# Optimization experiments

Measured on AMD Instinct MI355X. Metric: run time of the kernel, lower is better.

## Reference

```python
import jax, jax.numpy as jnp
import numpy as np

D_MODEL = 64
LN_EPS = 1e-5


def _conv1d(x, w, b, stride, pad):
    # x: (B, Cin, L), w: (Cout, Cin, K)
    y = jax.lax.conv_general_dilated(x, w, (stride,), [(pad, pad)],
                                     dimension_numbers=('NCH', 'OIH', 'NCH'))
    return y + b[None, :, None]


def _layernorm(x, g, b):
    # normalize over last dim (feature dim), matching nn.LayerNorm(d_model)
    m = jnp.mean(x, axis=-1, keepdims=True)
    v = jnp.var(x, axis=-1, keepdims=True)
    return (x - m) * jax.lax.rsqrt(v + LN_EPS) * g + b


def _pos_embed(L, d):
    pos = jnp.arange(L, dtype=jnp.float32)[:, None]
    div = jnp.exp(jnp.arange(0, d, 2, dtype=jnp.float32) * (-np.log(10000.0) / d))
    pe = jnp.zeros((L, d), jnp.float32)
    pe = pe.at[:, 0::2].set(jnp.sin(pos * div))
    pe = pe.at[:, 1::2].set(jnp.cos(pos * div))
    return pe


def setup_inputs():
    key = jax.random.key(0)
    ks = jax.random.split(key, 20)
    B, L, D = 128, 4096, D_MODEL
    G = D // 4  # 16 convs per kernel-size group (kernels cycle [3,5,7,9])
    inp = {'x': jax.random.normal(ks[0], (B, 1, L), jnp.float32)}
    kernels = [3, 5, 7, 9]
    for i, k in enumerate(kernels):
        fan = float(1.0 / np.sqrt(k))
        inp['tok_w%d' % k] = jax.random.uniform(ks[1 + 2 * i], (G, 1, k), jnp.float32, -fan, fan)
        inp['tok_b%d' % k] = jax.random.uniform(ks[2 + 2 * i], (G,), jnp.float32, -fan, fan)
    fan = float(1.0 / np.sqrt(D * 4))
    for j in range(3):
        inp['c_w%d' % (j + 1)] = jax.random.uniform(ks[10 + 2 * j], (D, D, 4), jnp.float32, -fan, fan)
        inp['c_b%d' % (j + 1)] = jax.random.uniform(ks[11 + 2 * j], (D,), jnp.float32, -fan, fan)
    for j in range(2):
        inp['ln_g%d' % (j + 1)] = jnp.ones((D,), jnp.float32)
        inp['ln_b%d' % (j + 1)] = jnp.zeros((D,), jnp.float32)
    return inp


def reference(x, tok_w3, tok_b3, tok_w5, tok_b5, tok_w7, tok_b7, tok_w9, tok_b9,
              c_w1, c_b1, c_w2, c_b2, c_w3, c_b3, ln_g1, ln_b1, ln_g2, ln_b2):
    B, _, L = x.shape
    D = D_MODEL
    # TokenEmbedding: conv i has kernel [3,5,7,9][i%4]; fuse the d_model 1-channel
    # convs into 4 grouped convs (one per kernel size), then interleave channels.
    outs = [
        _conv1d(x, tok_w3, tok_b3, 1, 1),
        _conv1d(x, tok_w5, tok_b5, 1, 2),
        _conv1d(x, tok_w7, tok_b7, 1, 3),
        _conv1d(x, tok_w9, tok_b9, 1, 4),
    ]  # each (B, D//4, L); group g holds channels i with i % 4 == g, ordered by i // 4
    emb = jnp.stack(outs, axis=2).reshape(B, D, L)  # channel i = (i//4)*4 + (i%4)
    # add sinusoidal positional embedding (dropout is identity in eval mode)
    h = emb + _pos_embed(L, D).T[None]  # (B, D, L)
    # CompressionEmbedding: conv(k=4, s=2, p=1) -> tanh -> LN (over D) chain
    h = jnp.tanh(_conv1d(h, c_w1, c_b1, 2, 1))
    h = _layernorm(h.transpose(0, 2, 1), ln_g1, ln_b1).transpose(0, 2, 1)
    h = jnp.tanh(_conv1d(h, c_w2, c_b2, 2, 1))
    h = _layernorm(h.transpose(0, 2, 1), ln_g2, ln_b2).transpose(0, 2, 1)
    h = jnp.tanh(_conv1d(h, c_w3, c_b3, 2, 1))
    return h.transpose(0, 2, 1)  # (B, L//8, D)
```

## Files before the change

kernel.cpp:

```cpp
#include <hip/hip_runtime.h>
#include <math.h>

#define BATCH 128
#define LN_EPS 1e-5f

typedef short bf16x8 __attribute__((ext_vector_type(8)));
typedef short bf16x4 __attribute__((ext_vector_type(4)));
typedef float f32x4  __attribute__((ext_vector_type(4)));

__device__ __forceinline__ ushort f2bf(float f) {
    return __builtin_bit_cast(ushort, (__bf16)f);
}

__device__ __forceinline__ float fast_tanh(float v) {
    float e = __expf(2.f * v);
    return 1.f - 2.f / (e + 1.f);
}

__global__ __launch_bounds__(256, 2)
void prep_kernel(const float* __restrict__ cw1, const float* __restrict__ cw2,
                 const float* __restrict__ cw3,
                 const float* __restrict__ w3, const float* __restrict__ b3,
                 const float* __restrict__ w5, const float* __restrict__ b5,
                 const float* __restrict__ w7, const float* __restrict__ b7,
                 const float* __restrict__ w9, const float* __restrict__ b9,
                 const float* __restrict__ cb1, const float* __restrict__ cb2,
                 const float* __restrict__ cb3,
                 const float* __restrict__ lg1, const float* __restrict__ lb1,
                 const float* __restrict__ lg2, const float* __restrict__ lb2,
                 ushort* __restrict__ Wm23, ushort* __restrict__ Wm1,
                 float* __restrict__ W0c, float* __restrict__ W3c,
                 float* __restrict__ pe1c,
                 float* __restrict__ cb2t, float* __restrict__ B2k0,
                 float* __restrict__ B2k3,
                 float* __restrict__ cb3t, float* __restrict__ B3k0,
                 float* __restrict__ B3k3) {
    const int tid = threadIdx.x;
    const int bx  = blockIdx.x;
    const int idx = bx * 256 + tid;

    __shared__ float tile[64][132];
    __shared__ float red[4][64][24];
    __shared__ float cbred[64][4];

    {
        int s = idx >> 14, r = idx & 16383;
        int j = r & 7, l15 = (r >> 3) & 15, dt = (r >> 7) & 3;
        int quad = (r >> 9) & 3, k2 = (r >> 11) & 1, kk = (r >> 12) & 3;
        int dout = dt * 16 + l15, din = k2 * 32 + quad * 8 + j;
        const float* cw = (s == 0) ? cw2 : cw3;
        const float* lg = (s == 0) ? lg1 : lg2;
        Wm23[idx] = f2bf(cw[dout * 256 + din * 4 + kk] * lg[din]);
    }

    if (bx == 1 && tid < 128) {
        const int s = tid >> 6, ch = tid & 63;
        const float* cw = (s == 0) ? cw2 : cw3;
        const float* lb = (s == 0) ? lb1 : lb2;
        float full = 0.f, k0 = 0.f, k3 = 0.f;
        for (int din = 0; din < 64; ++din) {
            float bv = lb[din];
            const float* wr = cw + ch * 256 + din * 4;
            k0 = fmaf(wr[0], bv, k0);
            k3 = fmaf(wr[3], bv, k3);
            full = fmaf(wr[0] + wr[1] + wr[2] + wr[3], bv, full);
        }
        if (s == 0) { cb2t[ch] = cb2[ch] + full; B2k0[ch] = k0; B2k3[ch] = k3; }
        else        { cb3t[ch] = cb3[ch] + full; B3k0[ch] = k0; B3k3[ch] = k3; }
    }

    if (bx == 0) {
        const int ch = tid & 63, part = tid >> 6;
        const float* cw1row = cw1 + ch * 256;
        float acc[24];
#pragma unroll
        for (int j = 0; j < 24; ++j) acc[j] = 0.f;
        for (int din = part * 16; din < part * 16 + 16; ++din) {
            int ki = din & 3, g = din >> 2;
            float wl[9];
#pragma unroll
            for (int j = 0; j < 9; ++j) wl[j] = 0.f;
            float bias;
            if (ki == 0)      { for (int j = 0; j < 3; ++j) wl[3 + j] = w3[g * 3 + j]; bias = b3[g]; }
            else if (ki == 1) { for (int j = 0; j < 5; ++j) wl[2 + j] = w5[g * 5 + j]; bias = b5[g]; }
            else if (ki == 2) { for (int j = 0; j < 7; ++j) wl[1 + j] = w7[g * 7 + j]; bias = b7[g]; }
            else              { for (int j = 0; j < 9; ++j) wl[j]     = w9[g * 9 + j]; bias = b9[g]; }
#pragma unroll
            for (int kk = 0; kk < 4; ++kk) {
                float c = cw1row[din * 4 + kk];
                acc[12 + kk] += c * bias;
#pragma unroll
                for (int u = 0; u < 9; ++u) acc[kk + u] += c * wl[u];
            }
            float c0 = cw1row[din * 4 + 0], c3 = cw1row[din * 4 + 3];
#pragma unroll
            for (int u = 0; u < 4; ++u) { acc[16 + u] += c0 * wl[5 + u]; acc[20 + u] += c3 * wl[u]; }
        }
#pragma unroll
        for (int j = 0; j < 24; ++j) red[part][ch][j] = acc[j];
    }

    {
        const int pair = tid & 63, part = tid >> 6;
        const int kk = pair >> 4, chl = pair & 15;
        const int ch = (bx & 3) * 16 + chl;
        float s = 0.f;
        for (int din = part * 16; din < part * 16 + 16; ++din) {
            int ki = din & 3, g = din >> 2;
            float bias = (ki == 0) ? b3[g] : (ki == 1) ? b5[g] : (ki == 2) ? b7[g] : b9[g];
            s += cw1[ch * 256 + din * 4 + kk] * bias;
        }
        cbred[pair][part] = s;
    }

    const int l0 = (bx >> 2) * 64;
    const int pin0 = 2 * l0 - 1;
    for (int i2 = tid; i2 < 64 * 130; i2 += 256) {
        int d = i2 / 130, pp = i2 - d * 130;
        int p = pin0 + pp;
        float v = 0.f;
        if (p >= 0 && p < 4096) {
            float dv = __expf((float)(d & ~1) * -0.14391156831212787f);
            float ang = (float)p * dv;
            v = (d & 1) ? __cosf(ang) : __sinf(ang);
        }
        tile[d][pp] = v;
    }
    __syncthreads();

    if (bx == 0 && tid < 64) {
        const int ch = tid;
        float w24[24];
#pragma unroll
        for (int j = 0; j < 24; ++j)
            w24[j] = red[0][ch][j] + red[1][ch][j] + red[2][ch][j] + red[3][ch][j];
        int dt = ch >> 4, l15 = ch & 15;
#pragma unroll
        for (int quad = 0; quad < 4; ++quad)
#pragma unroll
            for (int j = 0; j < 8; ++j) {
                int k = quad * 8 + j;
                Wm1[((quad * 4 + dt) * 16 + l15) * 8 + j] = f2bf(k < 12 ? w24[k] : 0.f);
            }
#pragma unroll
        for (int u = 0; u < 4; ++u) { W0c[ch * 4 + u] = w24[16 + u]; W3c[ch * 4 + u] = w24[20 + u]; }
    }

    const int lane = tid & 63, wv = tid >> 6;
    const int l = l0 + lane;
    const int chl0 = wv * 4;
    const int db = (bx & 3) * 16 + chl0;
    float a4[4];
#pragma unroll
    for (int j = 0; j < 4; ++j) {
        int chl = chl0 + j;
        float cbk0 = cbred[0 * 16 + chl][0] + cbred[0 * 16 + chl][1] + cbred[0 * 16 + chl][2] + cbred[0 * 16 + chl][3];
        float cbk1 = cbred[1 * 16 + chl][0] + cbred[1 * 16 + chl][1] + cbred[1 * 16 + chl][2] + cbred[1 * 16 + chl][3];
        float cbk2 = cbred[2 * 16 + chl][0] + cbred[2 * 16 + chl][1] + cbred[2 * 16 + chl][2] + cbred[2 * 16 + chl][3];
        float cbk3 = cbred[3 * 16 + chl][0] + cbred[3 * 16 + chl][1] + cbred[3 * 16 + chl][2] + cbred[3 * 16 + chl][3];
        float a = cb1[db + j] + cbk1 + cbk2;
        if (l > 0) a += cbk0;
        if (l < 2047) a += cbk3;
        a4[j] = a;
    }
    for (int din = 0; din < 64; ++din) {
        float v0 = tile[din][2 * lane + 0], v1 = tile[din][2 * lane + 1];
        float v2 = tile[din][2 * lane + 2], v3 = tile[din][2 * lane + 3];
        const float* wb = cw1 + din * 4;
#pragma unroll
        for (int j = 0; j < 4; ++j) {
            const float* wj = wb + (db + j) * 256;
            a4[j] = fmaf(v0, wj[0], fmaf(v1, wj[1], fmaf(v2, wj[2], fmaf(v3, wj[3], a4[j]))));
        }
    }
    *(float4*)(pe1c + (size_t)l * 64 + db) = make_float4(a4[0], a4[1], a4[2], a4[3]);
}

__global__ __launch_bounds__(256, 3)
void mega_kernel(const float* __restrict__ x,
                 const ushort* __restrict__ Wm1, const ushort* __restrict__ Wm23,
                 const float* __restrict__ pe1c,
                 const float* __restrict__ W0c, const float* __restrict__ W3c,
                 const float* __restrict__ cb2t, const float* __restrict__ B2k0,
                 const float* __restrict__ B2k3,
                 const float* __restrict__ cb3t, const float* __restrict__ B3k0,
                 const float* __restrict__ B3k3,
                 float* __restrict__ out) {
    const int b = blockIdx.y;
    const int g0 = blockIdx.x * 32;
    const int tid = threadIdx.x;

    __shared__ __align__(16) ushort xs[320];
    __shared__ __align__(16) ushort TE1[68][72];
    __shared__ __align__(16) ushort TO1[68][72];
    __shared__ __align__(16) ushort TE2[34][72];
    __shared__ __align__(16) ushort TO2[34][72];

    for (int i = tid; i < 320; i += 256) {
        int g = 8 * g0 - 11 + i;
        float v = (g >= 0 && g < 4096) ? x[b * 4096 + g] : 0.f;
        xs[i] = f2bf(v);
    }
    __syncthreads();

    const int wv = tid >> 6, lane = tid & 63;
    const int quad = lane >> 4, l15 = lane & 15;

    {
        bf16x8 afr1[4];
#pragma unroll
        for (int dt = 0; dt < 4; ++dt)
            afr1[dt] = *(const bf16x8*)&Wm1[((quad * 4 + dt) * 16 + l15) * 8];
        const int qstart = 4 * g0 - 3;
        for (int pass = wv; pass < 9; pass += 4) {
            const int m = pass * 16 + l15;
            const int q = qstart + m;
            const int qc = (q < 0) ? 0 : ((q > 2047) ? 2047 : q);
            f32x4 a1[4];
            const float* pb_ = pe1c + (size_t)qc * 64 + quad * 4;
#pragma unroll
            for (int dt = 0; dt < 4; ++dt) {
                float4 pv = *(const float4*)(pb_ + dt * 16);
                a1[dt][0] = pv.x; a1[dt][1] = pv.y; a1[dt][2] = pv.z; a1[dt][3] = pv.w;
            }
            union { bf16x8 v; unsigned u[4]; } tmp;
            const unsigned* p = (const unsigned*)&xs[2 * m + 8 * quad];
#pragma unroll
            for (int i = 0; i < 4; ++i) tmp.u[i] = p[i];
#pragma unroll
            for (int dt = 0; dt < 4; ++dt)
                a1[dt] = __builtin_amdgcn_mfma_f32_16x16x32_bf16(
                    afr1[dt], tmp.v, a1[dt], 0, 0, 0);
            if (m < 134) {
                ushort* dst = (m & 1) ? &TE1[(m + 1) >> 1][0] : &TO1[m >> 1][0];
                if (q >= 0 && q < 2048) {
                    if (q == 0 || q == 2047) {
                        const float* Wc = (q == 0) ? W0c : W3c;
                        const float* xe = x + b * 4096 + ((q == 0) ? 0 : 4092);
                        float x0 = xe[0], x1 = xe[1], x2 = xe[2], x3 = xe[3];
#pragma unroll
                        for (int dt = 0; dt < 4; ++dt)
#pragma unroll
                            for (int r = 0; r < 4; ++r) {
                                const float* wc = Wc + (dt * 16 + quad * 4 + r) * 4;
                                a1[dt][r] -= wc[0] * x0 + wc[1] * x1 + wc[2] * x2 + wc[3] * x3;
                            }
                    }
                    float s = 0.f, s2 = 0.f;
#pragma unroll
                    for (int dt = 0; dt < 4; ++dt)
#pragma unroll
                        for (int r = 0; r < 4; ++r) {
                            float t = fast_tanh(a1[dt][r]);
                            s += t;
                            s2 = fmaf(t, t, s2);
                        }
                    s += __shfl_xor(s, 16, 64);
                    s += __shfl_xor(s, 32, 64);
                    s2 += __shfl_xor(s2, 16, 64);
                    s2 += __shfl_xor(s2, 32, 64);
                    float mean = s * 0.015625f;
                    float var = fmaf(-mean, mean, s2 * 0.015625f);
                    float rstd = rsqrtf(var + LN_EPS);
                    float nmr = -mean * rstd;
#pragma unroll
                    for (int dt = 0; dt < 4; ++dt) {
                        bf16x4 pk;
#pragma unroll
                        for (int r = 0; r < 4; ++r)
                            pk[r] = (short)f2bf(fmaf(fast_tanh(a1[dt][r]), rstd, nmr));
                        *(bf16x4*)(dst + dt * 16 + quad * 4) = pk;
                    }
                } else {
                    bf16x4 z; z[0] = 0; z[1] = 0; z[2] = 0; z[3] = 0;
#pragma unroll
                    for (int dt = 0; dt < 4; ++dt)
                        *(bf16x4*)(dst + dt * 16 + quad * 4) = z;
                }
            }
        }
    }
    __syncthreads();

    for (int pass = wv; pass < 5; pass += 4) {
        const int n = pass * 16 + l15;
        const int nc = (n < 66) ? n : 65;
        f32x4 a2[4];
#pragma unroll
        for (int dt = 0; dt < 4; ++dt) {
            float4 cv = *(const float4*)(cb2t + dt * 16 + quad * 4);
            a2[dt][0] = cv.x; a2[dt][1] = cv.y; a2[dt][2] = cv.z; a2[dt][3] = cv.w;
        }
#pragma unroll
        for (int kk = 0; kk < 4; ++kk) {
            const ushort (*T)[72] = (kk & 1) ? TE1 : TO1;
            const int row = nc + ((kk + 1) >> 1);
#pragma unroll
            for (int k2 = 0; k2 < 2; ++k2) {
                bf16x8 bfr = *(const bf16x8*)&T[row][k2 * 32 + quad * 8];
                const ushort* wb = Wm23 + ((((kk * 2 + k2) * 4 + quad) * 4) * 16) * 8;
#pragma unroll
                for (int dt = 0; dt < 4; ++dt) {
                    bf16x8 afr = *(const bf16x8*)(wb + ((size_t)(dt * 16 + l15)) * 8);
                    a2[dt] = __builtin_amdgcn_mfma_f32_16x16x32_bf16(afr, bfr, a2[dt], 0, 0, 0);
                }
            }
        }
        if (n < 66) {
            const int p = 2 * g0 - 1 + n;
            ushort* dst = (n & 1) ? &TE2[(n + 1) >> 1][0] : &TO2[n >> 1][0];
            if (p >= 0 && p < 1024) {
                if (p == 0 || p == 1023) {
                    const float* Bc = (p == 0) ? B2k0 : B2k3;
#pragma unroll
                    for (int dt = 0; dt < 4; ++dt)
#pragma unroll
                        for (int r = 0; r < 4; ++r)
                            a2[dt][r] -= Bc[dt * 16 + quad * 4 + r];
                }
                float s = 0.f, s2 = 0.f;
#pragma unroll
                for (int dt = 0; dt < 4; ++dt)
#pragma unroll
                    for (int r = 0; r < 4; ++r) {
                        float t = fast_tanh(a2[dt][r]);
                        s += t;
                        s2 = fmaf(t, t, s2);
                    }
                s += __shfl_xor(s, 16, 64);
                s += __shfl_xor(s, 32, 64);
                s2 += __shfl_xor(s2, 16, 64);
                s2 += __shfl_xor(s2, 32, 64);
                float mean = s * 0.015625f;
                float var = fmaf(-mean, mean, s2 * 0.015625f);
                float rstd = rsqrtf(var + LN_EPS);
                float nmr = -mean * rstd;
#pragma unroll
                for (int dt = 0; dt < 4; ++dt) {
                    bf16x4 pk;
#pragma unroll
                    for (int r = 0; r < 4; ++r)
                        pk[r] = (short)f2bf(fmaf(fast_tanh(a2[dt][r]), rstd, nmr));
                    *(bf16x4*)(dst + dt * 16 + quad * 4) = pk;
                }
            } else {
                bf16x4 z; z[0] = 0; z[1] = 0; z[2] = 0; z[3] = 0;
#pragma unroll
                for (int dt = 0; dt < 4; ++dt)
                    *(bf16x4*)(dst + dt * 16 + quad * 4) = z;
            }
        }
    }
    __syncthreads();

    {
        const int m3 = (wv & 1) * 16 + l15;
        const int dth = wv >> 1;
        f32x4 a3[2];
#pragma unroll
        for (int d2 = 0; d2 < 2; ++d2) {
            float4 cv = *(const float4*)(cb3t + (dth * 2 + d2) * 16 + quad * 4);
            a3[d2][0] = cv.x; a3[d2][1] = cv.y; a3[d2][2] = cv.z; a3[d2][3] = cv.w;
        }
        const ushort* Wg3 = Wm23 + 16384;
#pragma unroll
        for (int kk = 0; kk < 4; ++kk) {
            const ushort (*T)[72] = (kk & 1) ? TE2 : TO2;
            const int row = m3 + ((kk + 1) >> 1);
#pragma unroll
            for (int k2 = 0; k2 < 2; ++k2) {
                bf16x8 bfr = *(const bf16x8*)&T[row][k2 * 32 + quad * 8];
                const ushort* wb = Wg3 + ((((kk * 2 + k2) * 4 + quad) * 4) * 16) * 8;
#pragma unroll
                for (int d2 = 0; d2 < 2; ++d2) {
                    const int dt = dth * 2 + d2;
                    bf16x8 afr = *(const bf16x8*)(wb + ((size_t)(dt * 16 + l15)) * 8);
                    a3[d2] = __builtin_amdgcn_mfma_f32_16x16x32_bf16(afr, bfr, a3[d2], 0, 0, 0);
                }
            }
        }
        const int l = g0 + m3;
        if (l == 0 || l == 511) {
            const float* Bc = (l == 0) ? B3k0 : B3k3;
#pragma unroll
            for (int d2 = 0; d2 < 2; ++d2)
#pragma unroll
                for (int r = 0; r < 4; ++r)
                    a3[d2][r] -= Bc[(dth * 2 + d2) * 16 + quad * 4 + r];
        }
        float* ob = out + ((size_t)(b * 512) + l) * 64;
#pragma unroll
        for (int d2 = 0; d2 < 2; ++d2) {
            const int dt = dth * 2 + d2;
            float4 st = make_float4(fast_tanh(a3[d2][0]),
                                    fast_tanh(a3[d2][1]),
                                    fast_tanh(a3[d2][2]),
                                    fast_tanh(a3[d2][3]));
            *(float4*)(ob + dt * 16 + quad * 4) = st;
        }
    }
}

extern "C" void kernel_launch(void* const* d_in, const int* in_sizes, int n_in,
                              void* d_out, int out_size, void* d_ws, size_t ws_size,
                              hipStream_t stream) {
    (void)in_sizes; (void)n_in; (void)out_size; (void)ws_size;
    const float* x   = (const float*)d_in[0];
    const float* w3  = (const float*)d_in[1];
    const float* b3  = (const float*)d_in[2];
    const float* w5  = (const float*)d_in[3];
    const float* b5  = (const float*)d_in[4];
    const float* w7  = (const float*)d_in[5];
    const float* b7  = (const float*)d_in[6];
    const float* w9  = (const float*)d_in[7];
    const float* b9  = (const float*)d_in[8];
    const float* cw1 = (const float*)d_in[9];
    const float* cb1 = (const float*)d_in[10];
    const float* cw2 = (const float*)d_in[11];
    const float* cb2 = (const float*)d_in[12];
    const float* cw3 = (const float*)d_in[13];
    const float* cb3 = (const float*)d_in[14];
    const float* lg1 = (const float*)d_in[15];
    const float* lb1 = (const float*)d_in[16];
    const float* lg2 = (const float*)d_in[17];
    const float* lb2 = (const float*)d_in[18];
    float* out = (float*)d_out;

    char* w = (char*)d_ws;
    ushort* Wm23 = (ushort*)(w + 0);
    ushort* Wm1  = (ushort*)(w + 65536);
    float*  W0c  = (float*)(w + 69632);
    float*  W3c  = (float*)(w + 70656);
    float*  cb2t = (float*)(w + 71680);
    float*  B2k0 = (float*)(w + 71936);
    float*  B2k3 = (float*)(w + 72192);
    float*  cb3t = (float*)(w + 72448);
    float*  B3k0 = (float*)(w + 72704);
    float*  B3k3 = (float*)(w + 72960);
    float*  pe1c = (float*)(w + 73216);

    prep_kernel<<<128, 256, 0, stream>>>(cw1, cw2, cw3, w3, b3, w5, b5, w7, b7, w9, b9,
                                         cb1, cb2, cb3, lg1, lb1, lg2, lb2,
                                         Wm23, Wm1, W0c, W3c, pe1c,
                                         cb2t, B2k0, B2k3, cb3t, B3k0, B3k3);
    mega_kernel<<<dim3(16, BATCH), 256, 0, stream>>>(
        x, Wm1, Wm23, pe1c, W0c, W3c, cb2t, B2k0, B2k3, cb3t, B3k0, B3k3, out);
}
```

Baseline: 170.1 us.

## Double mega-kernel tile to 64 output positions per block

Each block now processes 64 final positions instead of 32, with enlarged shared-memory tiles and stage loops that handle two 16-row MFMA tiles per pass in stage 1. This cuts the relative halo recomputation and lets stage 3 compute all 64 channels per wave. In exchange the grid halves, LDS use roughly doubles and launch bounds drop to 2 blocks per CU, which lowers occupancy.

```diff
diff --git a/kernel.cpp b/kernel.cpp
--- a/kernel.cpp
+++ b/kernel.cpp
@@ -176,7 +176,7 @@
     *(float4*)(pe1c + (size_t)l * 64 + db) = make_float4(a4[0], a4[1], a4[2], a4[3]);
 }
 
-__global__ __launch_bounds__(256, 3)
+__global__ __launch_bounds__(256, 2)
 void mega_kernel(const float* __restrict__ x,
                  const ushort* __restrict__ Wm1, const ushort* __restrict__ Wm23,
                  const float* __restrict__ pe1c,
@@ -187,16 +187,16 @@
                  const float* __restrict__ B3k3,
                  float* __restrict__ out) {
     const int b = blockIdx.y;
-    const int g0 = blockIdx.x * 32;
+    const int g0 = blockIdx.x * 64;
     const int tid = threadIdx.x;
 
-    __shared__ __align__(16) ushort xs[320];
-    __shared__ __align__(16) ushort TE1[68][72];
-    __shared__ __align__(16) ushort TO1[68][72];
-    __shared__ __align__(16) ushort TE2[34][72];
-    __shared__ __align__(16) ushort TO2[34][72];
-
-    for (int i = tid; i < 320; i += 256) {
+    __shared__ __align__(16) ushort xs[640];
+    __shared__ __align__(16) ushort TE1[148][72];
+    __shared__ __align__(16) ushort TO1[148][72];
+    __shared__ __align__(16) ushort TE2[66][72];
+    __shared__ __align__(16) ushort TO2[66][72];
+
+    for (int i = tid; i < 640; i += 256) {
         int g = 8 * g0 - 11 + i;
         float v = (g >= 0 && g < 4096) ? x[b * 4096 + g] : 0.f;
         xs[i] = f2bf(v);
@@ -213,25 +213,34 @@
             afr1[dt] = *(const bf16x8*)&Wm1[((quad * 4 + dt) * 16 + l15) * 8];
         const int qstart = 4 * g0 - 3;
         for (int pass = wv; pass < 9; pass += 4) {
-            const int m = pass * 16 + l15;
-            const int q = qstart + m;
-            const int qc = (q < 0) ? 0 : ((q > 2047) ? 2047 : q);
-            f32x4 a1[4];
-            const float* pb_ = pe1c + (size_t)qc * 64 + quad * 4;
-#pragma unroll
-            for (int dt = 0; dt < 4; ++dt) {
-                float4 pv = *(const float4*)(pb_ + dt * 16);
-                a1[dt][0] = pv.x; a1[dt][1] = pv.y; a1[dt][2] = pv.z; a1[dt][3] = pv.w;
-            }
-            union { bf16x8 v; unsigned u[4]; } tmp;
-            const unsigned* p = (const unsigned*)&xs[2 * m + 8 * quad];
-#pragma unroll
-            for (int i = 0; i < 4; ++i) tmp.u[i] = p[i];
-#pragma unroll
-            for (int dt = 0; dt < 4; ++dt)
-                a1[dt] = __builtin_amdgcn_mfma_f32_16x16x32_bf16(
-                    afr1[dt], tmp.v, a1[dt], 0, 0, 0);
-            if (m < 134) {
+            const int mb = pass * 32;
+            f32x4 a1[2][4];
+#pragma unroll
+            for (int pt = 0; pt < 2; ++pt) {
+                const int m = mb + pt * 16 + l15;
+                const int q = qstart + m;
+                const int qc = (q < 0) ? 0 : ((q > 2047) ? 2047 : q);
+                const float* pb_ = pe1c + (size_t)qc * 64 + quad * 4;
+#pragma unroll
+                for (int dt = 0; dt < 4; ++dt) {
+                    float4 pv = *(const float4*)(pb_ + dt * 16);
+                    a1[pt][dt][0] = pv.x; a1[pt][dt][1] = pv.y;
+                    a1[pt][dt][2] = pv.z; a1[pt][dt][3] = pv.w;
+                }
+                union { bf16x8 v; unsigned u[4]; } tmp;
+                const unsigned* p = (const unsigned*)&xs[2 * m + 8 * quad];
+#pragma unroll
+                for (int i = 0; i < 4; ++i) tmp.u[i] = p[i];
+#pragma unroll
+                for (int dt = 0; dt < 4; ++dt)
+                    a1[pt][dt] = __builtin_amdgcn_mfma_f32_16x16x32_bf16(
+                        afr1[dt], tmp.v, a1[pt][dt], 0, 0, 0);
+            }
+#pragma unroll
+            for (int pt = 0; pt < 2; ++pt) {
+                const int m = mb + pt * 16 + l15;
+                if (m >= 264) continue;
+                const int q = qstart + m;
                 ushort* dst = (m & 1) ? &TE1[(m + 1) >> 1][0] : &TO1[m >> 1][0];
                 if (q >= 0 && q < 2048) {
                     if (q == 0 || q == 2047) {
@@ -243,7 +252,7 @@
 #pragma unroll
                             for (int r = 0; r < 4; ++r) {
                                 const float* wc = Wc + (dt * 16 + quad * 4 + r) * 4;
-                                a1[dt][r] -= wc[0] * x0 + wc[1] * x1 + wc[2] * x2 + wc[3] * x3;
+                                a1[pt][dt][r] -= wc[0] * x0 + wc[1] * x1 + wc[2] * x2 + wc[3] * x3;
                             }
                     }
                     float s = 0.f, s2 = 0.f;
@@ -251,7 +260,7 @@
                     for (int dt = 0; dt < 4; ++dt)
 #pragma unroll
                         for (int r = 0; r < 4; ++r) {
-                            float t = fast_tanh(a1[dt][r]);
+                            float t = fast_tanh(a1[pt][dt][r]);
                             s += t;
                             s2 = fmaf(t, t, s2);
                         }
@@ -268,7 +277,7 @@
                         bf16x4 pk;
 #pragma unroll
                         for (int r = 0; r < 4; ++r)
-                            pk[r] = (short)f2bf(fmaf(fast_tanh(a1[dt][r]), rstd, nmr));
+                            pk[r] = (short)f2bf(fmaf(fast_tanh(a1[pt][dt][r]), rstd, nmr));
                         *(bf16x4*)(dst + dt * 16 + quad * 4) = pk;
                     }
                 } else {
@@ -282,9 +291,8 @@
     }
     __syncthreads();
 
-    for (int pass = wv; pass < 5; pass += 4) {
+    for (int pass = wv; pass < 9; pass += 4) {
         const int n = pass * 16 + l15;
-        const int nc = (n < 66) ? n : 65;
         f32x4 a2[4];
 #pragma unroll
         for (int dt = 0; dt < 4; ++dt) {
@@ -294,7 +302,7 @@
 #pragma unroll
         for (int kk = 0; kk < 4; ++kk) {
             const ushort (*T)[72] = (kk & 1) ? TE1 : TO1;
-            const int row = nc + ((kk + 1) >> 1);
+            const int row = n + ((kk + 1) >> 1);
 #pragma unroll
             for (int k2 = 0; k2 < 2; ++k2) {
                 bf16x8 bfr = *(const bf16x8*)&T[row][k2 * 32 + quad * 8];
@@ -306,7 +314,7 @@
                 }
             }
         }
-        if (n < 66) {
+        if (n < 130) {
             const int p = 2 * g0 - 1 + n;
             ushort* dst = (n & 1) ? &TE2[(n + 1) >> 1][0] : &TO2[n >> 1][0];
             if (p >= 0 && p < 1024) {
@@ -354,13 +362,12 @@
     __syncthreads();
 
     {
-        const int m3 = (wv & 1) * 16 + l15;
-        const int dth = wv >> 1;
-        f32x4 a3[2];
-#pragma unroll
-        for (int d2 = 0; d2 < 2; ++d2) {
-            float4 cv = *(const float4*)(cb3t + (dth * 2 + d2) * 16 + quad * 4);
-            a3[d2][0] = cv.x; a3[d2][1] = cv.y; a3[d2][2] = cv.z; a3[d2][3] = cv.w;
+        const int m3 = wv * 16 + l15;
+        f32x4 a3[4];
+#pragma unroll
+        for (int dt = 0; dt < 4; ++dt) {
+            float4 cv = *(const float4*)(cb3t + dt * 16 + quad * 4);
+            a3[dt][0] = cv.x; a3[dt][1] = cv.y; a3[dt][2] = cv.z; a3[dt][3] = cv.w;
         }
         const ushort* Wg3 = Wm23 + 16384;
 #pragma unroll
@@ -372,10 +379,9 @@
                 bf16x8 bfr = *(const bf16x8*)&T[row][k2 * 32 + quad * 8];
                 const ushort* wb = Wg3 + ((((kk * 2 + k2) * 4 + quad) * 4) * 16) * 8;
 #pragma unroll
-                for (int d2 = 0; d2 < 2; ++d2) {
-                    const int dt = dth * 2 + d2;
+                for (int dt = 0; dt < 4; ++dt) {
                     bf16x8 afr = *(const bf16x8*)(wb + ((size_t)(dt * 16 + l15)) * 8);
-                    a3[d2] = __builtin_amdgcn_mfma_f32_16x16x32_bf16(afr, bfr, a3[d2], 0, 0, 0);
+                    a3[dt] = __builtin_amdgcn_mfma_f32_16x16x32_bf16(afr, bfr, a3[dt], 0, 0, 0);
                 }
             }
         }
@@ -383,19 +389,18 @@
         if (l == 0 || l == 511) {
             const float* Bc = (l == 0) ? B3k0 : B3k3;
 #pragma unroll
-            for (int d2 = 0; d2 < 2; ++d2)
+            for (int dt = 0; dt < 4; ++dt)
 #pragma unroll
                 for (int r = 0; r < 4; ++r)
-                    a3[d2][r] -= Bc[(dth * 2 + d2) * 16 + quad * 4 + r];
+                    a3[dt][r] -= Bc[dt * 16 + quad * 4 + r];
         }
         float* ob = out + ((size_t)(b * 512) + l) * 64;
 #pragma unroll
-        for (int d2 = 0; d2 < 2; ++d2) {
-            const int dt = dth * 2 + d2;
-            float4 st = make_float4(fast_tanh(a3[d2][0]),
-                                    fast_tanh(a3[d2][1]),
-                                    fast_tanh(a3[d2][2]),
-                                    fast_tanh(a3[d2][3]));
+        for (int dt = 0; dt < 4; ++dt) {
+            float4 st = make_float4(fast_tanh(a3[dt][0]),
+                                    fast_tanh(a3[dt][1]),
+                                    fast_tanh(a3[dt][2]),
+                                    fast_tanh(a3[dt][3]));
             *(float4*)(ob + dt * 16 + quad * 4) = st;
         }
     }
@@ -443,6 +448,6 @@
                                          cb1, cb2, cb3, lg1, lb1, lg2, lb2,
                                          Wm23, Wm1, W0c, W3c, pe1c,
                                          cb2t, B2k0, B2k3, cb3t, B3k0, B3k3);
-    mega_kernel<<<dim3(16, BATCH), 256, 0, stream>>>(
+    mega_kernel<<<dim3(8, BATCH), 256, 0, stream>>>(
         x, Wm1, Wm23, pe1c, W0c, W3c, cb2t, B2k0, B2k3, cb3t, B3k0, B3k3, out);
 }
```

Measured after the change: 159.3 us. -6.4%, faster.
